# Optimization experiments

Measured on AMD Instinct MI355X. Metric: run time of the kernel, lower is better.

The kernel has to match this reference:

```python
import jax, jax.numpy as jnp
import numpy as np

N, L, T, F, H, E = 10000, 8, 16, 128, 256, 160000
NCONV = 3


def setup_inputs() -> dict:
    key = jax.random.key(0)
    ks = jax.random.split(key, 20)
    s = 0.05
    d = {}
    d['tree_inputs'] = jax.random.normal(ks[0], (N, L, F), jnp.float32)
    for i, name in enumerate(['seq2', 'seq3', 'seq4', 'seq5']):
        d[name] = jax.random.normal(ks[1 + i], (N, T, F), jnp.float32)
    d['edge_index'] = jax.random.randint(ks[5], (2, E), 0, N)
    d['tl_Wioux'] = jax.random.normal(ks[6], (3 * H, F)) * s
    d['tl_bioux'] = jnp.zeros((3 * H,))
    d['tl_Wiouh'] = jax.random.normal(ks[7], (3 * H, H)) * s
    d['tl_biouh'] = jnp.zeros((3 * H,))
    d['tl_Wfx'] = jax.random.normal(ks[8], (H, F)) * s
    d['tl_bfx'] = jnp.zeros((H,))
    d['tl_Wfh'] = jax.random.normal(ks[9], (H, H)) * s
    d['tl_bfh'] = jnp.zeros((H,))
    d['gru_Wih'] = jax.random.normal(ks[10], (4, 3 * H, F)) * s
    d['gru_Whh'] = jax.random.normal(ks[11], (4, 3 * H, H)) * s
    d['gru_bih'] = jnp.zeros((4, 3 * H))
    d['gru_bhh'] = jnp.zeros((4, 3 * H))
    d['comb_Wih'] = jax.random.normal(ks[12], (2, 3 * H, H)) * s
    d['comb_Whh'] = jax.random.normal(ks[13], (2, 3 * H, H)) * s
    d['comb_bih'] = jnp.zeros((2, 3 * H))
    d['comb_bhh'] = jnp.zeros((2, 3 * H))
    d['connect_W'] = jax.random.normal(ks[14], (H, 2 * 5 * H)) * s
    d['connect_b'] = jnp.zeros((H,))
    d['gcn_W'] = jax.random.normal(ks[15], (NCONV, H, H)) * s
    d['gcn_b'] = jnp.zeros((NCONV, H))
    return d


def _gru(x, Wih, Whh, bih, bhh, return_seq=False):
    # x: [N, T, F_in] -> last hidden [N, H] (or full seq [N, T, H])
    xg = jnp.einsum('ntf,gf->ntg', x, Wih) + bih  # precompute input projections
    h0 = jnp.zeros((x.shape[0], H), x.dtype)

    def step(h, xg_t):
        gh = h @ Whh.T + bhh
        r = jax.nn.sigmoid(xg_t[:, :H] + gh[:, :H])
        z = jax.nn.sigmoid(xg_t[:, H:2 * H] + gh[:, H:2 * H])
        n = jnp.tanh(xg_t[:, 2 * H:] + r * gh[:, 2 * H:])
        hn = (1.0 - z) * n + z * h
        return hn, (hn if return_seq else None)

    hT, ys = jax.lax.scan(step, h0, jnp.swapaxes(xg, 0, 1))
    return jnp.swapaxes(ys, 0, 1) if return_seq else hT


def reference(tree_inputs, seq2, seq3, seq4, seq5,
              tl_Wioux, tl_bioux, tl_Wiouh, tl_biouh, tl_Wfx, tl_bfx, tl_Wfh, tl_bfh,
              gru_Wih, gru_Whh, gru_bih, gru_bhh,
              comb_Wih, comb_Whh, comb_bih, comb_bhh,
              connect_W, connect_b, gcn_W, gcn_b, edge_index):
    # --- ChildSumTreeLSTM over chain trees (leaf -> root), vectorized over N trees ---
    xiou = jnp.einsum('nlf,gf->nlg', tree_inputs, tl_Wioux) + tl_bioux  # [N,L,3H]
    xf = jnp.einsum('nlf,hf->nlh', tree_inputs, tl_Wfx) + tl_bfx       # [N,L,H]

    def tstep(carry, inp):
        c, h = carry
        xiou_t, xf_t = inp
        iou = xiou_t + h @ tl_Wiouh.T + tl_biouh
        i = jax.nn.sigmoid(iou[:, :H])
        o = jax.nn.sigmoid(iou[:, H:2 * H])
        u = jnp.tanh(iou[:, 2 * H:])
        f = jax.nn.sigmoid(h @ tl_Wfh.T + tl_bfh + xf_t)
        c = i * u + f * c
        h = o * jnp.tanh(c)
        return (c, h), None

    c0 = jnp.zeros((N, H), tree_inputs.dtype)
    (_, feat1), _ = jax.lax.scan(tstep, (c0, c0), (jnp.swapaxes(xiou, 0, 1), jnp.swapaxes(xf, 0, 1)))

    # --- 4 unidirectional GRUs; keep last timestep (equal-length packed sequences) ---
    h2 = _gru(seq2, gru_Wih[0], gru_Whh[0], gru_bih[0], gru_bhh[0])
    h3 = _gru(seq3, gru_Wih[1], gru_Whh[1], gru_bih[1], gru_bhh[1])
    h4 = _gru(seq4, gru_Wih[2], gru_Whh[2], gru_bih[2], gru_bhh[2])
    h5 = _gru(seq5, gru_Wih[3], gru_Whh[3], gru_bih[3], gru_bhh[3])

    feats = jnp.stack([feat1, h2, h3, h4, h5], axis=1)  # [N,5,H]

    # --- bidirectional combine GRU ---
    out_f = _gru(feats, comb_Wih[0], comb_Whh[0], comb_bih[0], comb_bhh[0], return_seq=True)
    out_b = _gru(feats[:, ::-1, :], comb_Wih[1], comb_Whh[1], comb_bih[1], comb_bhh[1], return_seq=True)[:, ::-1, :]
    fv = jnp.concatenate([out_f, out_b], axis=-1).reshape(N, -1)  # [N, 5*2H]
    fv = fv @ connect_W.T + connect_b  # [N, H]  (dropout is identity at eval)

    # --- GCN layers (PyG GCNConv: add self-loops, symmetric norm) ---
    loops = jnp.arange(N)
    src = jnp.concatenate([edge_index[0], loops])
    dst = jnp.concatenate([edge_index[1], loops])
    deg = jax.ops.segment_sum(jnp.ones_like(src, fv.dtype), dst, num_segments=N)
    dinv = jax.lax.rsqrt(deg)  # deg >= 1 due to self-loops
    norm = dinv[src] * dinv[dst]

    def gcn(x, W, b):
        xw = x @ W.T
        agg = jax.ops.segment_sum(xw[src] * norm[:, None], dst, num_segments=N)
        return agg + b

    x = fv
    conv_output = x
    for i in range(NCONV):
        x = jax.nn.relu(gcn(x, gcn_W[i], gcn_b[i]))
        if i == NCONV - 1:
            # original code applies the last conv a second time for conv_output
            conv_output = jax.nn.relu(gcn(x, gcn_W[i], gcn_b[i]))

    pooled = jnp.max(conv_output, axis=0, keepdims=True)  # global max pool, single graph
    return pooled
```

## Files before the change

kernel.cpp:

```cpp
#include <hip/hip_runtime.h>
#include <math.h>

#define H 256
#define NROWS 10000
#define LTREE 8
#define TSEQ 16
#define FDIM 128
#define NE 160000
#define HTILE2 32768
#define XTILE 32768
#define H2 2621440
#define XZS 2621440

typedef __attribute__((ext_vector_type(8))) short short8;
typedef __attribute__((ext_vector_type(4))) float f32x4;
typedef unsigned short u16;

__device__ __forceinline__ u16 f2bf(float x) {
    unsigned int u = __float_as_uint(x);
    return (u16)((u + 0x7fffu + ((u >> 16) & 1u)) >> 16);
}
__device__ __forceinline__ float bf2f(u16 s) { return __uint_as_float(((unsigned int)s) << 16); }
__device__ __forceinline__ short8 ldf(const u16* __restrict__ p) { return *(const short8*)(p); }
__device__ __forceinline__ float fexp_(float x) { return __expf(fminf(x, 80.f)); }
__device__ __forceinline__ float fsig_(float x) { return 1.f / (1.f + fexp_(-x)); }
__device__ __forceinline__ float ftanh_(float x) {
    float e = fexp_(fmaxf(2.f * x, -80.f));
    return (e - 1.f) / (e + 1.f);
}
#define MFMA(A, B, C) C = __builtin_amdgcn_mfma_f32_16x16x32_bf16(A, B, C, 0, 0, 0)
#define MF2(AH, AL, BH, C) do { MFMA(AH, BH, C); MFMA(AL, BH, C); } while (0)

__device__ __forceinline__ void async16(u16* l, const u16* g) {
    __builtin_amdgcn_global_load_lds((__attribute__((address_space(1))) const void*)g,
                                     (__attribute__((address_space(3))) void*)l, 16, 0, 0);
}

__device__ __forceinline__ void xcd_swz(int& cbi, int& yy, int& zz) {
    const int gx = gridDim.x, gy = gridDim.y;
    int nwg8 = (gx * gy * gridDim.z) >> 3;
    int bid = blockIdx.x + gx * (blockIdx.y + gy * blockIdx.z);
    int wgid = (bid & 7) * nwg8 + (bid >> 3);
    cbi = wgid % gx;
    int rem = wgid / gx;
    yy = rem % gy;
    zz = rem / gy;
}

__device__ __forceinline__ size_t tpo128(int row, int g, int half) {
    return (size_t)(row >> 7) * XTILE + (size_t)(g >> 2) * 8192 +
           (size_t)((((g & 3) << 1) | half)) * 1024 + (size_t)(row & 127) * 8;
}
__device__ __forceinline__ size_t hpo(int row, int g) {
    return (size_t)(row >> 7) * HTILE2 + (size_t)g * 1024 + (size_t)(row & 127) * 8;
}

__device__ __forceinline__ void stageT(u16* ldsbuf, const u16* __restrict__ chunkbase,
                                       int w, int lane) {
#pragma unroll
    for (int cc = 0; cc < 4; cc++) {
        int eb = (w * 4 + cc) * 64;
        async16(ldsbuf + (size_t)eb * 8, chunkbase + (size_t)(eb + lane) * 8);
    }
}
__device__ __forceinline__ void stage64T(u16* ldsbuf, const u16* __restrict__ chunkbase,
                                         int w, int lane) {
#pragma unroll
    for (int cc = 0; cc < 2; cc++) {
        int p = w * 2 + cc;
        async16(ldsbuf + (size_t)p * 512, chunkbase + (size_t)p * 1024 + (size_t)lane * 8);
    }
}
__device__ __forceinline__ void stage_chunk64(u16* ldsbuf, const u16* __restrict__ src,
                                              int stride_u16, int kb_u16, int m0,
                                              int w, int lane) {
#pragma unroll
    for (int c = 0; c < 4; c++) {
        int e_base = (w * 4 + c) * 64;
        int e = e_base + lane;
        int p = e >> 6, rs = e & 63;
        int row = m0 + rs;
        if (row > NROWS - 1) row = NROWS - 1;
        const u16* g = src + (size_t)row * stride_u16 + kb_u16 + (p >> 1) * 16 + (p & 1) * 8;
        async16(ldsbuf + (size_t)e_base * 8, g);
    }
}

__device__ __forceinline__ void emit8t(u16* __restrict__ hi_p, u16* __restrict__ lo_p,
                                       const float* v8) {
    short8 h, l;
#pragma unroll
    for (int j = 0; j < 8; j++) {
        u16 hh = f2bf(v8[j]);
        h[j] = (short)hh;
        l[j] = (short)f2bf(v8[j] - bf2f(hh));
    }
    *(short8*)hi_p = h;
    *(short8*)(lo_p) = l;
}
__device__ __forceinline__ void emit8(u16* __restrict__ dst, const float* v8) {
    emit8t(dst, dst + 8, v8);
}
__global__ void k_splitWb(const float* __restrict__ src, u16* __restrict__ dst, int ngroups) {
    int g = blockIdx.x * 256 + threadIdx.x;
    if (g < ngroups) {
        float v[8];
        *(float4*)v = *(const float4*)(src + (size_t)g * 8);
        *(float4*)(v + 4) = *(const float4*)(src + (size_t)g * 8 + 4);
        short8 h;
#pragma unroll
        for (int j = 0; j < 8; j++) h[j] = (short)f2bf(v[j]);
        *(short8*)(dst + (size_t)g * 8) = h;
    }
}
__global__ void k_split_xseq(const float* __restrict__ s2, const float* __restrict__ s3,
                             const float* __restrict__ s4, const float* __restrict__ s5,
                             int t, u16* __restrict__ dst) {
    int bid = blockIdx.x;
    int xcd = bid & 7, chunk = bid >> 3;
    int z = xcd >> 1, half = xcd & 1;
    int g = chunk * 256 + threadIdx.x;
    int row = half * 5120 + (g >> 4);
    if (row >= NROWS) return;
    int gg = g & 15;
    const float* s = (z == 0) ? s2 : (z == 1) ? s3 : (z == 2) ? s4 : s5;
    const float* p = s + (size_t)row * (TSEQ * FDIM) + t * FDIM + gg * 8;
    float v[8];
    *(float4*)v = *(const float4*)p;
    *(float4*)(v + 4) = *(const float4*)(p + 4);
    u16* d = dst + (size_t)z * XZS;
    emit8t(d + tpo128(row, gg, 0), d + tpo128(row, gg, 1), v);
}
__global__ void k_split_xtree(const float* __restrict__ tree, int t, u16* __restrict__ dst) {
    int bid = blockIdx.x;
    int xcd = bid & 7, chunk = bid >> 3;
    int g = chunk * 256 + threadIdx.x;
    int row = xcd * 1280 + (g >> 4);
    if (row >= NROWS) return;
    int col = (g & 15) * 8;
    const float* p = tree + (size_t)row * (LTREE * FDIM) + t * FDIM + col;
    float v[8];
    *(float4*)v = *(const float4*)p;
    *(float4*)(v + 4) = *(const float4*)(p + 4);
    emit8(dst + (size_t)row * 256 + (size_t)(g & 15) * 16, v);
}
__global__ void k_splitNH2(const float* __restrict__ a, const float* __restrict__ b,
                           u16* __restrict__ dst) {
    int g = blockIdx.x * 256 + threadIdx.x;
    if (g < NROWS * 32) {
        float v[8];
        float4 x0 = *(const float4*)(a + (size_t)g * 8);
        float4 x1 = *(const float4*)(a + (size_t)g * 8 + 4);
        float4 y0 = *(const float4*)(b + (size_t)g * 8);
        float4 y1 = *(const float4*)(b + (size_t)g * 8 + 4);
        v[0] = x0.x + y0.x; v[1] = x0.y + y0.y; v[2] = x0.z + y0.z; v[3] = x0.w + y0.w;
        v[4] = x1.x + y1.x; v[5] = x1.y + y1.y; v[6] = x1.z + y1.z; v[7] = x1.w + y1.w;
        emit8(dst + (size_t)g * 16, v);
    }
}

template <int KX>
__global__ __launch_bounds__(256, 2) void k_rnn_step(
    const float* __restrict__ q0, const float* __restrict__ q1,
    const float* __restrict__ q2, const float* __restrict__ q3,
    int qoff4, u16* __restrict__ xnext,
    const u16* __restrict__ xp,
    const u16* __restrict__ Wih, long long wz,
    const u16* __restrict__ Whh, long long wzh,
    const float* __restrict__ bihB, const float* __restrict__ bhhB,
    const u16* __restrict__ hp,
    u16* __restrict__ op) {
    __shared__ u16 lds[2][8192];
    const int tid = threadIdx.x, lane = tid & 63, w = tid >> 6;
    const int lx = lane & 15, lg = lane >> 4;
    int cbi, yy, z;
    xcd_swz(cbi, yy, z);
    const int colw = cbi * 64 + w * 16;
    const int m0 = yy * 128;
    const u16* xb = xp + (size_t)z * XZS + (size_t)yy * XTILE;
    const u16* hb = hp + (size_t)z * H2;
    const u16* hbt = hb + (size_t)yy * HTILE2;
    const float* bih = bihB + z * 768;
    const float* bhh = bhhB + z * 768;
    constexpr int NCX = KX / 32;
    constexpr int NC = NCX + 4;

    const u16* bx0 = Wih + (size_t)z * wz + (size_t)(colw + lx) * KX + lg * 8;
    const u16* bx1 = bx0 + (size_t)256 * KX;
    const u16* bx2 = bx0 + (size_t)512 * KX;
    const u16* bh0 = Whh + (size_t)z * wzh + (size_t)(colw + lx) * 256 + lg * 8;
    const u16* bh1 = bh0 + 65536;
    const u16* bh2 = bh0 + 131072;

    const f32x4 zf = {0.f, 0.f, 0.f, 0.f};
    f32x4 aR[8], aZ[8], aNX[8], aNH[8];
#pragma unroll
    for (int rf = 0; rf < 8; rf++) { aR[rf] = zf; aZ[rf] = zf; aNX[rf] = zf; aNH[rf] = zf; }

    auto chunksrc = [&](int c) -> const u16* {
        return (c < NCX) ? xb + (size_t)c * 8192 : hbt + (size_t)(c - NCX) * 8192;
    };
    stageT(lds[0], chunksrc(0), w, lane);

    if (xnext) {
        const float* qs = (z == 0) ? q0 : (z == 1) ? q1 : (z == 2) ? q2 : q3;
        int row = m0 + (tid >> 1);
        if (row < NROWS) {
            int g0 = (cbi * 32 + (tid & 1) * 16) >> 3;
            const float* p = qs + (size_t)row * (TSEQ * FDIM) + qoff4 + g0 * 8;
            u16* d = xnext + (size_t)z * XZS;
            float v[8];
            *(float4*)v = *(const float4*)p;
            *(float4*)(v + 4) = *(const float4*)(p + 4);
            emit8t(d + tpo128(row, g0, 0), d + tpo128(row, g0, 1), v);
            *(float4*)v = *(const float4*)(p + 8);
            *(float4*)(v + 4) = *(const float4*)(p + 12);
            emit8t(d + tpo128(row, g0 + 1, 0), d + tpo128(row, g0 + 1, 1), v);
        }
    }

    for (int c = 0; c < NC; c++) {
        __syncthreads();
        if (c + 1 < NC) stageT(lds[(c + 1) & 1], chunksrc(c + 1), w, lane);
        const u16* lb = lds[c & 1];
        if (c < NCX) {
            short8 axh[8], axl[8];
            const u16* ph = lb + (size_t)(2 * lg) * 1024 + lx * 8;
#pragma unroll
            for (int rf = 0; rf < 8; rf++) {
                axh[rf] = ldf(ph + rf * 128);
                axl[rf] = ldf(ph + 1024 + rf * 128);
            }
            const int ko = c * 32;
            {
                short8 bh_ = ldf(bx0 + ko);
#pragma unroll
                for (int rf = 0; rf < 8; rf++) MF2(axh[rf], axl[rf], bh_, aR[rf]);
            }
            {
                short8 bh_ = ldf(bx1 + ko);
#pragma unroll
                for (int rf = 0; rf < 8; rf++) MF2(axh[rf], axl[rf], bh_, aZ[rf]);
            }
            {
                short8 bh_ = ldf(bx2 + ko);
#pragma unroll
                for (int rf = 0; rf < 8; rf++) MF2(axh[rf], axl[rf], bh_, aNX[rf]);
            }
        } else {
            const int cl = c - NCX;
#pragma unroll
            for (int s = 0; s < 2; s++) {
                short8 axh[8];
                const u16* ph = lb + (size_t)(s * 4 + lg) * 1024 + lx * 8;
#pragma unroll
                for (int rf = 0; rf < 8; rf++) axh[rf] = ldf(ph + rf * 128);
                const int ko = cl * 64 + s * 32;
                {
                    short8 bh_ = ldf(bh0 + ko);
#pragma unroll
                    for (int rf = 0; rf < 8; rf++) MFMA(axh[rf], bh_, aR[rf]);
                }
                {
                    short8 bh_ = ldf(bh1 + ko);
#pragma unroll
                    for (int rf = 0; rf < 8; rf++) MFMA(axh[rf], bh_, aZ[rf]);
                }
                {
                    short8 bh_ = ldf(bh2 + ko);
#pragma unroll
                    for (int rf = 0; rf < 8; rf++) MFMA(axh[rf], bh_, aNH[rf]);
                }
            }
        }
    }
    const int col = colw + lx;
    const float b_r = bih[col] + bhh[col];
    const float b_z = bih[256 + col] + bhh[256 + col];
    const float bx_n = bih[512 + col], bh_n = bhh[512 + col];
    const size_t colpart = (size_t)(col >> 3) * 1024 + (col & 7);
    u16* ob = op + (size_t)z * H2;
#pragma unroll
    for (int rf = 0; rf < 8; rf++) {
#pragma unroll
        for (int rr = 0; rr < 4; rr++) {
            int row = m0 + rf * 16 + lg * 4 + rr;
            if (row < NROWS) {
                float rg = fsig_(aR[rf][rr] + b_r);
                float zg = fsig_(aZ[rf][rr] + b_z);
                float ng = ftanh_(aNX[rf][rr] + bx_n + rg * (aNH[rf][rr] + bh_n));
                size_t addr = (size_t)(row >> 7) * HTILE2 + (size_t)(row & 127) * 8 + colpart;
                float hold = bf2f(hb[addr]);
                float hnew = (1.f - zg) * ng + zg * hold;
                ob[addr] = f2bf(hnew);
            }
        }
    }
}

__global__ __launch_bounds__(256, 3) void k_rnn_step64(
    const u16* __restrict__ xp, long long xo0, long long xo1,
    const u16* __restrict__ Wih, long long wz,
    const u16* __restrict__ Whh, long long wzh,
    const float* __restrict__ bihB, const float* __restrict__ bhhB,
    const u16* __restrict__ hp,
    u16* __restrict__ op) {
    __shared__ u16 lds[2][4096];
    const int tid = threadIdx.x, lane = tid & 63, w = tid >> 6;
    const int lx = lane & 15, lg = lane >> 4;
    int cbi, yy, z;
    xcd_swz(cbi, yy, z);
    const int colw = cbi * 64 + w * 16;
    const int m0 = yy * 64;
    const int tile = yy >> 1, rh = yy & 1;
    const u16* xb = xp + (size_t)((z == 1) ? xo1 : xo0) + (size_t)tile * HTILE2 + rh * 512;
    const u16* hb = hp + (size_t)z * H2;
    const u16* hbt = hb + (size_t)tile * HTILE2 + rh * 512;
    const float* bih = bihB + z * 768;
    const float* bhh = bhhB + z * 768;
    constexpr int NCX = 4, NC = 8;

    const u16* bx0 = Wih + (size_t)z * wz + (size_t)(colw + lx) * 256 + lg * 8;
    const u16* bx1 = bx0 + 65536;
    const u16* bx2 = bx0 + 131072;
    const u16* bh0 = Whh + (size_t)z * wzh + (size_t)(colw + lx) * 256 + lg * 8;
    const u16* bh1 = bh0 + 65536;
    const u16* bh2 = bh0 + 131072;

    const f32x4 zf = {0.f, 0.f, 0.f, 0.f};
    f32x4 aR[4], aZ[4], aNX[4], aNH[4];
#pragma unroll
    for (int rf = 0; rf < 4; rf++) { aR[rf] = zf; aZ[rf] = zf; aNX[rf] = zf; aNH[rf] = zf; }

    auto chunksrc = [&](int c) -> const u16* {
        return (c < NCX) ? xb + (size_t)c * 8192 : hbt + (size_t)(c - NCX) * 8192;
    };
    stage64T(lds[0], chunksrc(0), w, lane);

    for (int c = 0; c < NC; c++) {
        __syncthreads();
        if (c + 1 < NC) stage64T(lds[(c + 1) & 1], chunksrc(c + 1), w, lane);
        const u16* lb = lds[c & 1];
        const bool isX = (c < NCX);
        const int cl = isX ? c : c - NCX;
#pragma unroll
        for (int s = 0; s < 2; s++) {
            short8 axh[4];
            const u16* ph = lb + (size_t)(s * 4 + lg) * 512 + lx * 8;
#pragma unroll
            for (int rf = 0; rf < 4; rf++) axh[rf] = ldf(ph + rf * 128);
            const int ko = cl * 64 + s * 32;
            if (isX) {
                {
                    short8 bh_ = ldf(bx0 + ko);
#pragma unroll
                    for (int rf = 0; rf < 4; rf++) MFMA(axh[rf], bh_, aR[rf]);
                }
                {
                    short8 bh_ = ldf(bx1 + ko);
#pragma unroll
                    for (int rf = 0; rf < 4; rf++) MFMA(axh[rf], bh_, aZ[rf]);
                }
                {
                    short8 bh_ = ldf(bx2 + ko);
#pragma unroll
                    for (int rf = 0; rf < 4; rf++) MFMA(axh[rf], bh_, aNX[rf]);
                }
            } else {
                {
                    short8 bh_ = ldf(bh0 + ko);
#pragma unroll
                    for (int rf = 0; rf < 4; rf++) MFMA(axh[rf], bh_, aR[rf]);
                }
                {
                    short8 bh_ = ldf(bh1 + ko);
#pragma unroll
                    for (int rf = 0; rf < 4; rf++) MFMA(axh[rf], bh_, aZ[rf]);
                }
                {
                    short8 bh_ = ldf(bh2 + ko);
#pragma unroll
                    for (int rf = 0; rf < 4; rf++) MFMA(axh[rf], bh_, aNH[rf]);
                }
            }
        }
    }
    const int col = colw + lx;
    const float b_r = bih[col] + bhh[col];
    const float b_z = bih[256 + col] + bhh[256 + col];
    const float bx_n = bih[512 + col], bh_n = bhh[512 + col];
    const size_t colpart = (size_t)(col >> 3) * 1024 + (col & 7);
    u16* ob = op + (size_t)z * H2;
#pragma unroll
    for (int rf = 0; rf < 4; rf++) {
#pragma unroll
        for (int rr = 0; rr < 4; rr++) {
            int row = m0 + rf * 16 + lg * 4 + rr;
            if (row < NROWS) {
                float rg = fsig_(aR[rf][rr] + b_r);
                float zg = fsig_(aZ[rf][rr] + b_z);
                float ng = ftanh_(aNX[rf][rr] + bx_n + rg * (aNH[rf][rr] + bh_n));
                size_t addr = (size_t)(row >> 7) * HTILE2 + (size_t)(row & 127) * 8 + colpart;
                float hold = bf2f(hb[addr]);
                float hnew = (1.f - zg) * ng + zg * hold;
                ob[addr] = f2bf(hnew);
            }
        }
    }
}

__global__ __launch_bounds__(256, 3) void k_tree_step_mf(
    const float* __restrict__ treenext, u16* __restrict__ xtnext,
    const u16* __restrict__ txp,
    const u16* __restrict__ Wx, const u16* __restrict__ Wh,
    const u16* __restrict__ Wfx, const u16* __restrict__ Wfh,
    const float* __restrict__ bioux, const float* __restrict__ biouh,
    const float* __restrict__ bfx, const float* __restrict__ bfh,
    const u16* __restrict__ hp, float* __restrict__ cst,
    u16* __restrict__ op, int tiledOut) {
    __shared__ u16 lds[2][8192];
    const int tid = threadIdx.x, lane = tid & 63, w = tid >> 6;
    const int lx = lane & 15, lg = lane >> 4;
    int cbi, yy, zz;
    xcd_swz(cbi, yy, zz);
    const int colw = cbi * 64 + w * 16;
    const int m0 = yy * 64;
    constexpr int NCX = 2, NC = 6;

    const u16* bx0 = Wx + (size_t)(colw + lx) * 128 + lg * 8;
    const u16* bx1 = bx0 + 32768;
    const u16* bx2 = bx0 + 65536;
    const u16* bxf = Wfx + (size_t)(colw + lx) * 128 + lg * 8;
    const u16* bh0 = Wh + (size_t)(colw + lx) * 256 + lg * 8;
    const u16* bh1 = bh0 + 65536;
    const u16* bh2 = bh0 + 131072;
    const u16* bhf = Wfh + (size_t)(colw + lx) * 256 + lg * 8;

    const f32x4 zf = {0.f, 0.f, 0.f, 0.f};
    f32x4 aI[4], aO[4], aU[4], aF[4];
#pragma unroll
    for (int rf = 0; rf < 4; rf++) { aI[rf] = zf; aO[rf] = zf; aU[rf] = zf; aF[rf] = zf; }

    stage_chunk64(lds[0], txp, 256, 0, m0, w, lane);

    if (xtnext) {
        int row = m0 + (tid >> 2);
        if (row < NROWS) {
            int c0 = cbi * 32 + (tid & 3) * 8;
            const float* p = treenext + (size_t)row * (LTREE * FDIM) + c0;
            float v[8];
            *(float4*)v = *(const float4*)p;
            *(float4*)(v + 4) = *(const float4*)(p + 4);
            emit8(xtnext + (size_t)row * 256 + (size_t)(c0 >> 3) * 16, v);
        }
    }

    for (int c = 0; c < NC; c++) {
        __syncthreads();
        if (c + 1 < NC) {
            u16* nb = lds[(c + 1) & 1];
            if (c + 1 < NCX) stage_chunk64(nb, txp, 256, (c + 1) * 128, m0, w, lane);
            else stage_chunk64(nb, hp, 512, (c + 1 - NCX) * 128, m0, w, lane);
        }
        const u16* lb = lds[c & 1];
        const bool isX = (c < NCX);
        const int cl = isX ? c : c - NCX;
#pragma unroll
        for (int s = 0; s < 2; s++) {
            short8 axh[4], axl[4];
            const u16* ph = lb + (size_t)(2 * (s * 4 + lg)) * 512 + lx * 8;
#pragma unroll
            for (int rf = 0; rf < 4; rf++) {
                axh[rf] = ldf(ph + rf * 128);
                axl[rf] = ldf(ph + 512 + rf * 128);
            }
            const int ko = cl * 64 + s * 32;
            const u16* p0 = isX ? bx0 : bh0;
            const u16* p1 = isX ? bx1 : bh1;
            const u16* p2 = isX ? bx2 : bh2;
            const u16* p3 = isX ? bxf : bhf;
            {
                short8 bh_ = ldf(p0 + ko);
#pragma unroll
                for (int rf = 0; rf < 4; rf++) MF2(axh[rf], axl[rf], bh_, aI[rf]);
            }
            {
                short8 bh_ = ldf(p1 + ko);
#pragma unroll
                for (int rf = 0; rf < 4; rf++) MF2(axh[rf], axl[rf], bh_, aO[rf]);
            }
            {
                short8 bh_ = ldf(p2 + ko);
#pragma unroll
                for (int rf = 0; rf < 4; rf++) MF2(axh[rf], axl[rf], bh_, aU[rf]);
            }
            {
                short8 bh_ = ldf(p3 + ko);
#pragma unroll
                for (int rf = 0; rf < 4; rf++) MF2(axh[rf], axl[rf], bh_, aF[rf]);
            }
        }
    }
    const int col = colw + lx;
    const float b_i = bioux[col] + biouh[col];
    const float b_o = bioux[256 + col] + biouh[256 + col];
    const float b_u = bioux[512 + col] + biouh[512 + col];
    const float b_f = bfx[col] + bfh[col];
    const int cpo = ((col >> 3) << 4) + (col & 7);
    const size_t colpart2 = (size_t)(col >> 3) * 1024 + (col & 7);
#pragma unroll
    for (int rf = 0; rf < 4; rf++) {
#pragma unroll
        for (int rr = 0; rr < 4; rr++) {
            int row = m0 + rf * 16 + lg * 4 + rr;
            if (row < NROWS) {
                float ig = fsig_(aI[rf][rr] + b_i);
                float og = fsig_(aO[rf][rr] + b_o);
                float ug = ftanh_(aU[rf][rr] + b_u);
                float fg = fsig_(aF[rf][rr] + b_f);
                size_t ci = (size_t)row * H + col;
                float cnew = ig * ug + fg * cst[ci];
                cst[ci] = cnew;
                float hnew = og * ftanh_(cnew);
                if (tiledOut) {
                    size_t addr = (size_t)(row >> 7) * HTILE2 + (size_t)(row & 127) * 8 + colpart2;
                    op[addr] = f2bf(hnew);
                } else {
                    u16 hh = f2bf(hnew);
                    size_t oi = (size_t)row * 512 + cpo;
                    op[oi] = hh;
                    op[oi + 8] = f2bf(hnew - bf2f(hh));
                }
            }
        }
    }
}

__global__ __launch_bounds__(256) void k_fv_acc_mf(
    float* __restrict__ fvbase, const u16* __restrict__ hq,
    const u16* __restrict__ Wc, int off_f, int off_b) {
    const int tid = threadIdx.x, lane = tid & 63, w = tid >> 6;
    const int lx = lane & 15, kl8 = (lane >> 4);
    int cbi, yy, z;
    xcd_swz(cbi, yy, z);
    const int wr = w >> 1, wc = w & 1;
    const int cb = cbi * 64 + wc * 32;
    const int m0 = yy * 128 + wr * 64;
    int arow[4];
#pragma unroll
    for (int rf = 0; rf < 4; rf++) {
        int r = m0 + rf * 16 + lx;
        arow[rf] = (r < NROWS) ? r : NROWS - 1;
    }
    const f32x4 zf = {0.f, 0.f, 0.f, 0.f};
    f32x4 acc[4][2] = {{zf, zf}, {zf, zf}, {zf, zf}, {zf, zf}};
    const u16* aB = hq + (size_t)z * H2;
    const int off = z ? off_b : off_f;
    const u16* a[4];
#pragma unroll
    for (int rf = 0; rf < 4; rf++) {
        a[rf] = aB + (size_t)(arow[rf] >> 7) * HTILE2 + (size_t)(arow[rf] & 127) * 8 +
                (size_t)kl8 * 1024;
    }
    const u16* bp0 = Wc + (size_t)(cb + lx) * 2560 + off + kl8 * 8;
    const u16* bp1 = bp0 + 16 * 2560;
#pragma unroll
    for (int it = 0; it < 8; it++) {
        short8 axh[4];
#pragma unroll
        for (int rf = 0; rf < 4; rf++) {
            axh[rf] = ldf(a[rf]);
            a[rf] += 4096;
        }
        const int kb = it * 32;
        {
            short8 bh = ldf(bp0 + kb);
#pragma unroll
            for (int rf = 0; rf < 4; rf++) MFMA(axh[rf], bh, acc[rf][0]);
        }
        {
            short8 bh = ldf(bp1 + kb);
#pragma unroll
            for (int rf = 0; rf < 4; rf++) MFMA(axh[rf], bh, acc[rf][1]);
        }
    }
    float* fv = fvbase + (size_t)z * (NROWS * H);
#pragma unroll
    for (int rf = 0; rf < 4; rf++) {
#pragma unroll
        for (int cf = 0; cf < 2; cf++) {
            int col = cb + cf * 16 + lx;
#pragma unroll
            for (int rr = 0; rr < 4; rr++) {
                int row = m0 + rf * 16 + (lane >> 4) * 4 + rr;
                if (row < NROWS) fv[(size_t)row * H + col] += acc[rf][cf][rr];
            }
        }
    }
}

__global__ __launch_bounds__(256) void k_gcn_gemm(
    float* __restrict__ out, const u16* __restrict__ ap_, const u16* __restrict__ W) {
    const int tid = threadIdx.x, lane = tid & 63, w = tid >> 6;
    const int lx = lane & 15, kl = (lane >> 4) * 8;
    int cbi, yy, zz;
    xcd_swz(cbi, yy, zz);
    const int cb = cbi * 64, m0 = yy * 128 + w * 32;
    int arow[2];
#pragma unroll
    for (int rf = 0; rf < 2; rf++) {
        int r = m0 + rf * 16 + lx;
        arow[rf] = (r < NROWS) ? r : NROWS - 1;
    }
    const f32x4 zf = {0.f, 0.f, 0.f, 0.f};
    f32x4 acc[2][4] = {{zf, zf, zf, zf}, {zf, zf, zf, zf}};
    const u16* a0 = ap_ + (size_t)arow[0] * 512 + kl * 2;
    const u16* a1 = ap_ + (size_t)arow[1] * 512 + kl * 2;
    const u16* bp0 = W + (size_t)(cb + lx) * 256 + kl;
    const u16* bp1 = bp0 + 16 * 256;
    const u16* bp2 = bp0 + 32 * 256;
    const u16* bp3 = bp0 + 48 * 256;
#pragma unroll
    for (int kb = 0; kb < 256; kb += 32) {
        short8 axh[2], axl[2];
        axh[0] = ldf(a0 + kb * 2); axl[0] = ldf(a0 + kb * 2 + 8);
        axh[1] = ldf(a1 + kb * 2); axl[1] = ldf(a1 + kb * 2 + 8);
        {
            short8 bh = ldf(bp0 + kb);
#pragma unroll
            for (int rf = 0; rf < 2; rf++) MF2(axh[rf], axl[rf], bh, acc[rf][0]);
        }
        {
            short8 bh = ldf(bp1 + kb);
#pragma unroll
            for (int rf = 0; rf < 2; rf++) MF2(axh[rf], axl[rf], bh, acc[rf][1]);
        }
        {
            short8 bh = ldf(bp2 + kb);
#pragma unroll
            for (int rf = 0; rf < 2; rf++) MF2(axh[rf], axl[rf], bh, acc[rf][2]);
        }
        {
            short8 bh = ldf(bp3 + kb);
#pragma unroll
            for (int rf = 0; rf < 2; rf++) MF2(axh[rf], axl[rf], bh, acc[rf][3]);
        }
    }
#pragma unroll
    for (int rf = 0; rf < 2; rf++) {
#pragma unroll
        for (int cf = 0; cf < 4; cf++) {
            int col = cb + cf * 16 + lx;
#pragma unroll
            for (int rr = 0; rr < 4; rr++) {
                int row = m0 + rf * 16 + (lane >> 4) * 4 + rr;
                if (row < NROWS) out[(size_t)row * H + col] = acc[rf][cf][rr];
            }
        }
    }
}

__global__ void k_fv_init(float* fv, const float* __restrict__ b) {
    int idx = blockIdx.x * 256 + threadIdx.x;
    if (idx < NROWS * H) fv[idx] = b[idx & (H - 1)];
}
__global__ void k_cnt(int* __restrict__ cnt, const int* __restrict__ dst) {
    int i = blockIdx.x * 256 + threadIdx.x;
    if (i < NE) atomicAdd(&cnt[dst[i]], 1);
}
__global__ void k_scan(const int* __restrict__ cnt, int* __restrict__ rowptr) {
    __shared__ int part[256];
    int tid = threadIdx.x;
    int st = tid * 40, en = (st + 40 > NROWS) ? NROWS : st + 40;
    int s = 0;
    for (int i = st; i < en; i++) s += cnt[i];
    part[tid] = s;
    __syncthreads();
    if (tid == 0) {
        int run = 0;
        for (int i = 0; i < 256; i++) { int t = part[i]; part[i] = run; run += t; }
        rowptr[NROWS] = run;
    }
    __syncthreads();
    int run = part[tid];
    for (int i = st; i < en; i++) { rowptr[i] = run; run += cnt[i]; }
}
__global__ void k_dinv(float* __restrict__ dinv, const int* __restrict__ cnt) {
    int i = blockIdx.x * 256 + threadIdx.x;
    if (i < NROWS) dinv[i] = rsqrtf(1.0f + (float)cnt[i]);
}
__global__ void k_fill(int* __restrict__ csr, int* __restrict__ cursor,
                       const int* __restrict__ rowptr, const int* __restrict__ ei) {
    int e = blockIdx.x * 256 + threadIdx.x;
    if (e < NE) {
        int d = ei[NE + e];
        int p = atomicAdd(&cursor[d], 1);
        csr[rowptr[d] + p] = ei[e];
    }
}
__global__ __launch_bounds__(256) void k_gather(
    float* __restrict__ out, u16* __restrict__ xcp,
    const float* __restrict__ xw, const float* __restrict__ dinv,
    const int* __restrict__ rowptr, const int* __restrict__ csr, const float* __restrict__ b) {
    int node = blockIdx.x * 4 + (threadIdx.x >> 6);
    if (node >= NROWS) return;
    int lane = threadIdx.x & 63;
    float dn = dinv[node];
    float4 acc = *(const float4*)(xw + (size_t)node * H + lane * 4);
    float dn2 = dn * dn;
    acc.x *= dn2; acc.y *= dn2; acc.z *= dn2; acc.w *= dn2;
    int e0 = rowptr[node], e1 = rowptr[node + 1];
    for (int i = e0; i < e1; i++) {
        int s = csr[i];
        float wgt = dn * dinv[s];
        const float4 v = *(const float4*)(xw + (size_t)s * H + lane * 4);
        acc.x += v.x * wgt; acc.y += v.y * wgt; acc.z += v.z * wgt; acc.w += v.w * wgt;
    }
    const float4 bv = *(const float4*)(b + lane * 4);
    float o[4];
    o[0] = fmaxf(acc.x + bv.x, 0.f);
    o[1] = fmaxf(acc.y + bv.y, 0.f);
    o[2] = fmaxf(acc.z + bv.z, 0.f);
    o[3] = fmaxf(acc.w + bv.w, 0.f);
    *(float4*)(out + (size_t)node * H + lane * 4) = *(const float4*)o;
    u16 hs[4], ls[4];
#pragma unroll
    for (int j = 0; j < 4; j++) {
        hs[j] = f2bf(o[j]);
        ls[j] = f2bf(o[j] - bf2f(hs[j]));
    }
    size_t bidx = (size_t)node * 512 + (size_t)(lane >> 1) * 16 + (lane & 1) * 4;
    *(short4*)(xcp + bidx) = *(const short4*)hs;
    *(short4*)(xcp + bidx + 8) = *(const short4*)ls;
}
__global__ void k_colmax(float* __restrict__ out, const float* __restrict__ x) {
    int j = threadIdx.x;
    float m = 0.0f;
    for (int r = blockIdx.x; r < NROWS; r += gridDim.x)
        m = fmaxf(m, x[(size_t)r * H + j]);
    atomicMax((int*)&out[j], __float_as_int(m));
}

extern "C" void kernel_launch(void* const* d_in, const int* in_sizes, int n_in,
                              void* d_out, int out_size, void* d_ws, size_t ws_size,
                              hipStream_t stream) {
    const float* tree = (const float*)d_in[0];
    const float* s2 = (const float*)d_in[1];
    const float* s3 = (const float*)d_in[2];
    const float* s4 = (const float*)d_in[3];
    const float* s5 = (const float*)d_in[4];
    const int* edge = (const int*)d_in[5];
    const float* tl_Wioux = (const float*)d_in[6];
    const float* tl_bioux = (const float*)d_in[7];
    const float* tl_Wiouh = (const float*)d_in[8];
    const float* tl_biouh = (const float*)d_in[9];
    const float* tl_Wfx = (const float*)d_in[10];
    const float* tl_bfx = (const float*)d_in[11];
    const float* tl_Wfh = (const float*)d_in[12];
    const float* tl_bfh = (const float*)d_in[13];
    const float* gru_Wih = (const float*)d_in[14];
    const float* gru_Whh = (const float*)d_in[15];
    const float* gru_bih = (const float*)d_in[16];
    const float* gru_bhh = (const float*)d_in[17];
    const float* comb_Wih = (const float*)d_in[18];
    const float* comb_Whh = (const float*)d_in[19];
    const float* comb_bih = (const float*)d_in[20];
    const float* comb_bhh = (const float*)d_in[21];
    const float* connect_W = (const float*)d_in[22];
    const float* connect_b = (const float*)d_in[23];
    const float* gcn_W = (const float*)d_in[24];
    const float* gcn_b = (const float*)d_in[25];

    char* base = (char*)d_ws;
    size_t off = 0;
    auto aus = [&](size_t nu16) { u16* p = (u16*)(base + off); off += nu16 * sizeof(u16); return p; };
    u16* tx = aus(98304);
    u16* th = aus(196608);
    u16* tfx = aus(32768);
    u16* tfh = aus(65536);
    u16* gWih = aus(393216);
    u16* gWhh = aus(786432);
    u16* cWih = aus(393216);
    u16* cWhh = aus(393216);
    u16* cn = aus(655360);
    u16* gc = aus(196608);
    u16* feats = aus((size_t)5 * H2);
    u16* hA = aus((size_t)4 * H2);
    u16* hB = aus((size_t)4 * H2);
    u16* SA = aus((size_t)4 * XZS);
    u16* SB = aus((size_t)4 * XZS);

    const dim3 blk(256);

    hipMemsetAsync(d_out, 0, H * sizeof(float), stream);

    auto SPW = [&](const float* s, u16* d, int n) {
        k_splitWb<<<(n / 8 + 255) / 256, blk, 0, stream>>>(s, d, n / 8);
    };
    SPW(tl_Wioux, tx, 98304);
    SPW(tl_Wiouh, th, 196608);
    SPW(tl_Wfx, tfx, 32768);
    SPW(tl_Wfh, tfh, 65536);
    SPW(gru_Wih, gWih, 393216);
    SPW(gru_Whh, gWhh, 786432);
    SPW(comb_Wih, cWih, 393216);
    SPW(comb_Whh, cWhh, 393216);
    SPW(connect_W, cn, 655360);
    SPW(gcn_W, gc, 196608);

    float* cbuf = (float*)SA;
    u16* xtA = SA + 5120000;
    u16* xtB = SA + 7680000;
    hipMemsetAsync(hA, 0, (size_t)NROWS * 512 * 2, stream);
    hipMemsetAsync(cbuf, 0, (size_t)NROWS * H * 4, stream);
    k_split_xtree<<<640, blk, 0, stream>>>(tree, 0, xtA);
    {
        u16 *p = hA, *q = hB;
        for (int t = 0; t < LTREE; ++t) {
            bool last = (t == LTREE - 1);
            u16* xin = (t & 1) ? xtB : xtA;
            u16* xnx = last ? (u16*)0 : ((t & 1) ? xtA : xtB);
            k_tree_step_mf<<<dim3(4, 160, 1), blk, 0, stream>>>(
                tree + (t + 1) * FDIM, xnx,
                xin, tx, th, tfx, tfh, tl_bioux, tl_biouh, tl_bfx, tl_bfh,
                p, cbuf, last ? feats : q, last ? 1 : 0);
            u16* tmp = p; p = q; q = tmp;
        }
    }

    u16* xsA = SA;
    u16* xsB = SB;
    hipMemsetAsync(hA, 0, (size_t)4 * H2 * 2, stream);
    k_split_xseq<<<2560, blk, 0, stream>>>(s2, s3, s4, s5, 0, xsA);
    {
        u16 *p = hA, *q = hB;
        for (int t = 0; t < TSEQ; ++t) {
            bool last = (t == TSEQ - 1);
            u16* xin = (t & 1) ? xsB : xsA;
            u16* xnx = last ? (u16*)0 : ((t & 1) ? xsA : xsB);
            k_rnn_step<128><<<dim3(4, 80, 4), blk, 0, stream>>>(
                s2, s3, s4, s5, (t + 1) * FDIM, xnx,
                xin,
                gWih, 98304LL, gWhh, 196608LL, gru_bih, gru_bhh,
                p,
                last ? feats + H2 : q);
            u16* tmp = p; p = q; q = tmp;
        }
    }

    float* fvF = (float*)SA;
    float* fvB = fvF + (size_t)NROWS * H;
    hipMemsetAsync(hA, 0, (size_t)2 * H2 * 2, stream);
    k_fv_init<<<(NROWS * H + 255) / 256, blk, 0, stream>>>(fvF, connect_b);
    hipMemsetAsync(fvB, 0, (size_t)NROWS * H * 4, stream);
    {
        u16 *p = hA, *q = hB;
        for (int s = 0; s < 5; ++s) {
            k_rnn_step64<<<dim3(4, 160, 2), blk, 0, stream>>>(
                feats, (long long)s * H2, (long long)(4 - s) * H2,
                cWih, 196608LL, cWhh, 196608LL, comb_bih, comb_bhh,
                p, q);
            k_fv_acc_mf<<<dim3(4, 79, 2), blk, 0, stream>>>(
                fvF, q, cn, s * 512, (4 - s) * 512 + 256);
            u16* tmp = p; p = q; q = tmp;
        }
    }

    int* cnt = (int*)(hB + 6000000);
    int* rowptr = cnt + 10016;
    int* cursor = rowptr + 10016;
    int* csr = cursor + 10016;
    float* dinv = (float*)(csr + NE);
    hipMemsetAsync(cnt, 0, NROWS * sizeof(int), stream);
    hipMemsetAsync(cursor, 0, NROWS * sizeof(int), stream);
    k_cnt<<<(NE + 255) / 256, blk, 0, stream>>>(cnt, edge + NE);
    k_scan<<<1, blk, 0, stream>>>(cnt, rowptr);
    k_dinv<<<(NROWS + 255) / 256, blk, 0, stream>>>(dinv, cnt);
    k_fill<<<(NE + 255) / 256, blk, 0, stream>>>(csr, cursor, rowptr, edge);

    {
        u16* xc = hB;
        float* xw = (float*)SB;
        float* cur = fvF;
        float* nxt = (float*)hA;
        k_splitNH2<<<1250, blk, 0, stream>>>(fvF, fvB, xc);
        for (int i = 0; i < 4; ++i) {
            int wi = (i < 3) ? i : 2;
            k_gcn_gemm<<<dim3(4, 80, 1), blk, 0, stream>>>(xw, xc, gc + (size_t)wi * 65536);
            k_gather<<<(NROWS + 3) / 4, blk, 0, stream>>>(nxt, xc, xw, dinv, rowptr, csr,
                                                          gcn_b + wi * H);
            float* tmp = cur; cur = nxt; nxt = tmp;
        }
        k_colmax<<<256, blk, 0, stream>>>((float*)d_out, cur);
    }
}
```

Before: 1.932 ms.

## Drop split-bf16 hi/lo activation encoding, use single bf16 operands everywhere

Removes the hi+lo two-term bf16 representation of activations (x inputs, tree hidden state, GCN inputs), which doubled MFMA count and operand bytes for those products. Buffers, layouts, staging helpers and the MFMA loops are rewritten for a single bf16 term, halving the chunk count for input projections and the memory traffic for these activations. The cost is lower precision in the matmuls, which may push results closer to or past the tolerance.

```diff
diff --git a/kernel.cpp b/kernel.cpp
--- a/kernel.cpp
+++ b/kernel.cpp
@@ -8,9 +8,9 @@
 #define FDIM 128
 #define NE 160000
 #define HTILE2 32768
-#define XTILE 32768
+#define XT2 16384
 #define H2 2621440
-#define XZS 2621440
+#define XZ2 1310720
 
 typedef __attribute__((ext_vector_type(8))) short short8;
 typedef __attribute__((ext_vector_type(4))) float f32x4;
@@ -29,7 +29,6 @@
     return (e - 1.f) / (e + 1.f);
 }
 #define MFMA(A, B, C) C = __builtin_amdgcn_mfma_f32_16x16x32_bf16(A, B, C, 0, 0, 0)
-#define MF2(AH, AL, BH, C) do { MFMA(AH, BH, C); MFMA(AL, BH, C); } while (0)
 
 __device__ __forceinline__ void async16(u16* l, const u16* g) {
     __builtin_amdgcn_global_load_lds((__attribute__((address_space(1))) const void*)g,
@@ -47,12 +46,8 @@
     zz = rem / gy;
 }
 
-__device__ __forceinline__ size_t tpo128(int row, int g, int half) {
-    return (size_t)(row >> 7) * XTILE + (size_t)(g >> 2) * 8192 +
-           (size_t)((((g & 3) << 1) | half)) * 1024 + (size_t)(row & 127) * 8;
-}
-__device__ __forceinline__ size_t hpo(int row, int g) {
-    return (size_t)(row >> 7) * HTILE2 + (size_t)g * 1024 + (size_t)(row & 127) * 8;
+__device__ __forceinline__ size_t xpo(int row, int g) {
+    return (size_t)(row >> 7) * XT2 + (size_t)g * 1024 + (size_t)(row & 127) * 8;
 }
 
 __device__ __forceinline__ void stageT(u16* ldsbuf, const u16* __restrict__ chunkbase,
@@ -71,9 +66,9 @@
         async16(ldsbuf + (size_t)p * 512, chunkbase + (size_t)p * 1024 + (size_t)lane * 8);
     }
 }
-__device__ __forceinline__ void stage_chunk64(u16* ldsbuf, const u16* __restrict__ src,
-                                              int stride_u16, int kb_u16, int m0,
-                                              int w, int lane) {
+__device__ __forceinline__ void stage_chunk64h(u16* ldsbuf, const u16* __restrict__ src,
+                                               int stride_u16, int kb_u16, int m0,
+                                               int w, int lane) {
 #pragma unroll
     for (int c = 0; c < 4; c++) {
         int e_base = (w * 4 + c) * 64;
@@ -81,25 +76,16 @@
         int p = e >> 6, rs = e & 63;
         int row = m0 + rs;
         if (row > NROWS - 1) row = NROWS - 1;
-        const u16* g = src + (size_t)row * stride_u16 + kb_u16 + (p >> 1) * 16 + (p & 1) * 8;
+        const u16* g = src + (size_t)row * stride_u16 + kb_u16 + p * 8;
         async16(ldsbuf + (size_t)e_base * 8, g);
     }
 }
 
-__device__ __forceinline__ void emit8t(u16* __restrict__ hi_p, u16* __restrict__ lo_p,
-                                       const float* v8) {
-    short8 h, l;
-#pragma unroll
-    for (int j = 0; j < 8; j++) {
-        u16 hh = f2bf(v8[j]);
-        h[j] = (short)hh;
-        l[j] = (short)f2bf(v8[j] - bf2f(hh));
-    }
-    *(short8*)hi_p = h;
-    *(short8*)(lo_p) = l;
-}
-__device__ __forceinline__ void emit8(u16* __restrict__ dst, const float* v8) {
-    emit8t(dst, dst + 8, v8);
+__device__ __forceinline__ void emit8h(u16* __restrict__ dst, const float* v8) {
+    short8 h;
+#pragma unroll
+    for (int j = 0; j < 8; j++) h[j] = (short)f2bf(v8[j]);
+    *(short8*)dst = h;
 }
 __global__ void k_splitWb(const float* __restrict__ src, u16* __restrict__ dst, int ngroups) {
     int g = blockIdx.x * 256 + threadIdx.x;
@@ -107,10 +93,7 @@
         float v[8];
         *(float4*)v = *(const float4*)(src + (size_t)g * 8);
         *(float4*)(v + 4) = *(const float4*)(src + (size_t)g * 8 + 4);
-        short8 h;
-#pragma unroll
-        for (int j = 0; j < 8; j++) h[j] = (short)f2bf(v[j]);
-        *(short8*)(dst + (size_t)g * 8) = h;
+        emit8h(dst + (size_t)g * 8, v);
     }
 }
 __global__ void k_split_xseq(const float* __restrict__ s2, const float* __restrict__ s3,
@@ -128,8 +111,7 @@
     float v[8];
     *(float4*)v = *(const float4*)p;
     *(float4*)(v + 4) = *(const float4*)(p + 4);
-    u16* d = dst + (size_t)z * XZS;
-    emit8t(d + tpo128(row, gg, 0), d + tpo128(row, gg, 1), v);
+    emit8h(dst + (size_t)z * XZ2 + xpo(row, gg), v);
 }
 __global__ void k_split_xtree(const float* __restrict__ tree, int t, u16* __restrict__ dst) {
     int bid = blockIdx.x;
@@ -142,7 +124,7 @@
     float v[8];
     *(float4*)v = *(const float4*)p;
     *(float4*)(v + 4) = *(const float4*)(p + 4);
-    emit8(dst + (size_t)row * 256 + (size_t)(g & 15) * 16, v);
+    emit8h(dst + (size_t)row * 128 + col, v);
 }
 __global__ void k_splitNH2(const float* __restrict__ a, const float* __restrict__ b,
                            u16* __restrict__ dst) {
@@ -155,11 +137,10 @@
         float4 y1 = *(const float4*)(b + (size_t)g * 8 + 4);
         v[0] = x0.x + y0.x; v[1] = x0.y + y0.y; v[2] = x0.z + y0.z; v[3] = x0.w + y0.w;
         v[4] = x1.x + y1.x; v[5] = x1.y + y1.y; v[6] = x1.z + y1.z; v[7] = x1.w + y1.w;
-        emit8(dst + (size_t)g * 16, v);
-    }
-}
-
-template <int KX>
+        emit8h(dst + (size_t)g * 8, v);
+    }
+}
+
 __global__ __launch_bounds__(256, 2) void k_rnn_step(
     const float* __restrict__ q0, const float* __restrict__ q1,
     const float* __restrict__ q2, const float* __restrict__ q3,
@@ -177,17 +158,16 @@
     xcd_swz(cbi, yy, z);
     const int colw = cbi * 64 + w * 16;
     const int m0 = yy * 128;
-    const u16* xb = xp + (size_t)z * XZS + (size_t)yy * XTILE;
+    const u16* xb = xp + (size_t)z * XZ2 + (size_t)yy * XT2;
     const u16* hb = hp + (size_t)z * H2;
     const u16* hbt = hb + (size_t)yy * HTILE2;
     const float* bih = bihB + z * 768;
     const float* bhh = bhhB + z * 768;
-    constexpr int NCX = KX / 32;
-    constexpr int NC = NCX + 4;
-
-    const u16* bx0 = Wih + (size_t)z * wz + (size_t)(colw + lx) * KX + lg * 8;
-    const u16* bx1 = bx0 + (size_t)256 * KX;
-    const u16* bx2 = bx0 + (size_t)512 * KX;
+    constexpr int NCX = 2, NC = 6;
+
+    const u16* bx0 = Wih + (size_t)z * wz + (size_t)(colw + lx) * 128 + lg * 8;
+    const u16* bx1 = bx0 + 32768;
+    const u16* bx2 = bx0 + 65536;
     const u16* bh0 = Whh + (size_t)z * wzh + (size_t)(colw + lx) * 256 + lg * 8;
     const u16* bh1 = bh0 + 65536;
     const u16* bh2 = bh0 + 131072;
@@ -208,14 +188,14 @@
         if (row < NROWS) {
             int g0 = (cbi * 32 + (tid & 1) * 16) >> 3;
             const float* p = qs + (size_t)row * (TSEQ * FDIM) + qoff4 + g0 * 8;
-            u16* d = xnext + (size_t)z * XZS;
+            u16* d = xnext + (size_t)z * XZ2;
             float v[8];
             *(float4*)v = *(const float4*)p;
             *(float4*)(v + 4) = *(const float4*)(p + 4);
-            emit8t(d + tpo128(row, g0, 0), d + tpo128(row, g0, 1), v);
+            emit8h(d + xpo(row, g0), v);
             *(float4*)v = *(const float4*)(p + 8);
             *(float4*)(v + 4) = *(const float4*)(p + 12);
-            emit8t(d + tpo128(row, g0 + 1, 0), d + tpo128(row, g0 + 1, 1), v);
+            emit8h(d + xpo(row, g0 + 1), v);
         }
     }
 
@@ -223,39 +203,32 @@
         __syncthreads();
         if (c + 1 < NC) stageT(lds[(c + 1) & 1], chunksrc(c + 1), w, lane);
         const u16* lb = lds[c & 1];
-        if (c < NCX) {
-            short8 axh[8], axl[8];
-            const u16* ph = lb + (size_t)(2 * lg) * 1024 + lx * 8;
-#pragma unroll
-            for (int rf = 0; rf < 8; rf++) {
-                axh[rf] = ldf(ph + rf * 128);
-                axl[rf] = ldf(ph + 1024 + rf * 128);
-            }
-            const int ko = c * 32;
-            {
-                short8 bh_ = ldf(bx0 + ko);
-#pragma unroll
-                for (int rf = 0; rf < 8; rf++) MF2(axh[rf], axl[rf], bh_, aR[rf]);
-            }
-            {
-                short8 bh_ = ldf(bx1 + ko);
-#pragma unroll
-                for (int rf = 0; rf < 8; rf++) MF2(axh[rf], axl[rf], bh_, aZ[rf]);
-            }
-            {
-                short8 bh_ = ldf(bx2 + ko);
-#pragma unroll
-                for (int rf = 0; rf < 8; rf++) MF2(axh[rf], axl[rf], bh_, aNX[rf]);
-            }
-        } else {
-            const int cl = c - NCX;
-#pragma unroll
-            for (int s = 0; s < 2; s++) {
-                short8 axh[8];
-                const u16* ph = lb + (size_t)(s * 4 + lg) * 1024 + lx * 8;
-#pragma unroll
-                for (int rf = 0; rf < 8; rf++) axh[rf] = ldf(ph + rf * 128);
-                const int ko = cl * 64 + s * 32;
+        const bool isX = (c < NCX);
+        const int cl = isX ? c : c - NCX;
+#pragma unroll
+        for (int s = 0; s < 2; s++) {
+            short8 axh[8];
+            const u16* ph = lb + (size_t)(s * 4 + lg) * 1024 + lx * 8;
+#pragma unroll
+            for (int rf = 0; rf < 8; rf++) axh[rf] = ldf(ph + rf * 128);
+            const int ko = cl * 64 + s * 32;
+            if (isX) {
+                {
+                    short8 bh_ = ldf(bx0 + ko);
+#pragma unroll
+                    for (int rf = 0; rf < 8; rf++) MFMA(axh[rf], bh_, aR[rf]);
+                }
+                {
+                    short8 bh_ = ldf(bx1 + ko);
+#pragma unroll
+                    for (int rf = 0; rf < 8; rf++) MFMA(axh[rf], bh_, aZ[rf]);
+                }
+                {
+                    short8 bh_ = ldf(bx2 + ko);
+#pragma unroll
+                    for (int rf = 0; rf < 8; rf++) MFMA(axh[rf], bh_, aNX[rf]);
+                }
+            } else {
                 {
                     short8 bh_ = ldf(bh0 + ko);
 #pragma unroll
@@ -425,7 +398,7 @@
     xcd_swz(cbi, yy, zz);
     const int colw = cbi * 64 + w * 16;
     const int m0 = yy * 64;
-    constexpr int NCX = 2, NC = 6;
+    constexpr int NC = 3;
 
     const u16* bx0 = Wx + (size_t)(colw + lx) * 128 + lg * 8;
     const u16* bx1 = bx0 + 32768;
@@ -441,7 +414,7 @@
 #pragma unroll
     for (int rf = 0; rf < 4; rf++) { aI[rf] = zf; aO[rf] = zf; aU[rf] = zf; aF[rf] = zf; }
 
-    stage_chunk64(lds[0], txp, 256, 0, m0, w, lane);
+    stage_chunk64h(lds[0], txp, 128, 0, m0, w, lane);
 
     if (xtnext) {
         int row = m0 + (tid >> 2);
@@ -451,30 +424,22 @@
             float v[8];
             *(float4*)v = *(const float4*)p;
             *(float4*)(v + 4) = *(const float4*)(p + 4);
-            emit8(xtnext + (size_t)row * 256 + (size_t)(c0 >> 3) * 16, v);
+            emit8h(xtnext + (size_t)row * 128 + c0, v);
         }
     }
 
     for (int c = 0; c < NC; c++) {
         __syncthreads();
-        if (c + 1 < NC) {
-            u16* nb = lds[(c + 1) & 1];
-            if (c + 1 < NCX) stage_chunk64(nb, txp, 256, (c + 1) * 128, m0, w, lane);
-            else stage_chunk64(nb, hp, 512, (c + 1 - NCX) * 128, m0, w, lane);
-        }
+        if (c + 1 < NC) stage_chunk64h(lds[(c + 1) & 1], hp, 256, c * 128, m0, w, lane);
         const u16* lb = lds[c & 1];
-        const bool isX = (c < NCX);
-        const int cl = isX ? c : c - NCX;
-#pragma unroll
-        for (int s = 0; s < 2; s++) {
-            short8 axh[4], axl[4];
-            const u16* ph = lb + (size_t)(2 * (s * 4 + lg)) * 512 + lx * 8;
-#pragma unroll
-            for (int rf = 0; rf < 4; rf++) {
-                axh[rf] = ldf(ph + rf * 128);
-                axl[rf] = ldf(ph + 512 + rf * 128);
-            }
-            const int ko = cl * 64 + s * 32;
+        const bool isX = (c == 0);
+#pragma unroll
+        for (int s = 0; s < 4; s++) {
+            short8 axh[4];
+            const u16* ph = lb + (size_t)(s * 4 + lg) * 512 + lx * 8;
+#pragma unroll
+            for (int rf = 0; rf < 4; rf++) axh[rf] = ldf(ph + rf * 128);
+            const int ko = isX ? s * 32 : (c - 1) * 128 + s * 32;
             const u16* p0 = isX ? bx0 : bh0;
             const u16* p1 = isX ? bx1 : bh1;
             const u16* p2 = isX ? bx2 : bh2;
@@ -482,22 +447,22 @@
             {
                 short8 bh_ = ldf(p0 + ko);
 #pragma unroll
-                for (int rf = 0; rf < 4; rf++) MF2(axh[rf], axl[rf], bh_, aI[rf]);
+                for (int rf = 0; rf < 4; rf++) MFMA(axh[rf], bh_, aI[rf]);
             }
             {
                 short8 bh_ = ldf(p1 + ko);
 #pragma unroll
-                for (int rf = 0; rf < 4; rf++) MF2(axh[rf], axl[rf], bh_, aO[rf]);
+                for (int rf = 0; rf < 4; rf++) MFMA(axh[rf], bh_, aO[rf]);
             }
             {
                 short8 bh_ = ldf(p2 + ko);
 #pragma unroll
-                for (int rf = 0; rf < 4; rf++) MF2(axh[rf], axl[rf], bh_, aU[rf]);
+                for (int rf = 0; rf < 4; rf++) MFMA(axh[rf], bh_, aU[rf]);
             }
             {
                 short8 bh_ = ldf(p3 + ko);
 #pragma unroll
-                for (int rf = 0; rf < 4; rf++) MF2(axh[rf], axl[rf], bh_, aF[rf]);
+                for (int rf = 0; rf < 4; rf++) MFMA(axh[rf], bh_, aF[rf]);
             }
         }
     }
@@ -506,7 +471,6 @@
     const float b_o = bioux[256 + col] + biouh[256 + col];
     const float b_u = bioux[512 + col] + biouh[512 + col];
     const float b_f = bfx[col] + bfh[col];
-    const int cpo = ((col >> 3) << 4) + (col & 7);
     const size_t colpart2 = (size_t)(col >> 3) * 1024 + (col & 7);
 #pragma unroll
     for (int rf = 0; rf < 4; rf++) {
@@ -526,10 +490,7 @@
                     size_t addr = (size_t)(row >> 7) * HTILE2 + (size_t)(row & 127) * 8 + colpart2;
                     op[addr] = f2bf(hnew);
                 } else {
-                    u16 hh = f2bf(hnew);
-                    size_t oi = (size_t)row * 512 + cpo;
-                    op[oi] = hh;
-                    op[oi + 8] = f2bf(hnew - bf2f(hh));
+                    op[(size_t)row * 256 + col] = f2bf(hnew);
                 }
             }
         }
@@ -614,36 +575,36 @@
     }
     const f32x4 zf = {0.f, 0.f, 0.f, 0.f};
     f32x4 acc[2][4] = {{zf, zf, zf, zf}, {zf, zf, zf, zf}};
-    const u16* a0 = ap_ + (size_t)arow[0] * 512 + kl * 2;
-    const u16* a1 = ap_ + (size_t)arow[1] * 512 + kl * 2;
+    const u16* a0 = ap_ + (size_t)arow[0] * 256 + kl;
+    const u16* a1 = ap_ + (size_t)arow[1] * 256 + kl;
     const u16* bp0 = W + (size_t)(cb + lx) * 256 + kl;
     const u16* bp1 = bp0 + 16 * 256;
     const u16* bp2 = bp0 + 32 * 256;
     const u16* bp3 = bp0 + 48 * 256;
 #pragma unroll
     for (int kb = 0; kb < 256; kb += 32) {
-        short8 axh[2], axl[2];
-        axh[0] = ldf(a0 + kb * 2); axl[0] = ldf(a0 + kb * 2 + 8);
-        axh[1] = ldf(a1 + kb * 2); axl[1] = ldf(a1 + kb * 2 + 8);
+        short8 axh[2];
+        axh[0] = ldf(a0 + kb);
+        axh[1] = ldf(a1 + kb);
         {
             short8 bh = ldf(bp0 + kb);
 #pragma unroll
-            for (int rf = 0; rf < 2; rf++) MF2(axh[rf], axl[rf], bh, acc[rf][0]);
+            for (int rf = 0; rf < 2; rf++) MFMA(axh[rf], bh, acc[rf][0]);
         }
         {
             short8 bh = ldf(bp1 + kb);
 #pragma unroll
-            for (int rf = 0; rf < 2; rf++) MF2(axh[rf], axl[rf], bh, acc[rf][1]);
+            for (int rf = 0; rf < 2; rf++) MFMA(axh[rf], bh, acc[rf][1]);
         }
         {
             short8 bh = ldf(bp2 + kb);
 #pragma unroll
-            for (int rf = 0; rf < 2; rf++) MF2(axh[rf], axl[rf], bh, acc[rf][2]);
+            for (int rf = 0; rf < 2; rf++) MFMA(axh[rf], bh, acc[rf][2]);
         }
         {
             short8 bh = ldf(bp3 + kb);
 #pragma unroll
-            for (int rf = 0; rf < 2; rf++) MF2(axh[rf], axl[rf], bh, acc[rf][3]);
+            for (int rf = 0; rf < 2; rf++) MFMA(axh[rf], bh, acc[rf][3]);
         }
     }
 #pragma unroll
@@ -723,15 +684,10 @@
     o[2] = fmaxf(acc.z + bv.z, 0.f);
     o[3] = fmaxf(acc.w + bv.w, 0.f);
     *(float4*)(out + (size_t)node * H + lane * 4) = *(const float4*)o;
-    u16 hs[4], ls[4];
-#pragma unroll
-    for (int j = 0; j < 4; j++) {
-        hs[j] = f2bf(o[j]);
-        ls[j] = f2bf(o[j] - bf2f(hs[j]));
-    }
-    size_t bidx = (size_t)node * 512 + (size_t)(lane >> 1) * 16 + (lane & 1) * 4;
-    *(short4*)(xcp + bidx) = *(const short4*)hs;
-    *(short4*)(xcp + bidx + 8) = *(const short4*)ls;
+    u16 hs[4];
+#pragma unroll
+    for (int j = 0; j < 4; j++) hs[j] = f2bf(o[j]);
+    *(short4*)(xcp + (size_t)node * 256 + lane * 4) = *(const short4*)hs;
 }
 __global__ void k_colmax(float* __restrict__ out, const float* __restrict__ x) {
     int j = threadIdx.x;
@@ -787,8 +743,8 @@
     u16* feats = aus((size_t)5 * H2);
     u16* hA = aus((size_t)4 * H2);
     u16* hB = aus((size_t)4 * H2);
-    u16* SA = aus((size_t)4 * XZS);
-    u16* SB = aus((size_t)4 * XZS);
+    u16* SA = aus((size_t)8 * XZ2);
+    u16* SB = aus((size_t)8 * XZ2);
 
     const dim3 blk(256);
 
@@ -810,8 +766,8 @@
 
     float* cbuf = (float*)SA;
     u16* xtA = SA + 5120000;
-    u16* xtB = SA + 7680000;
-    hipMemsetAsync(hA, 0, (size_t)NROWS * 512 * 2, stream);
+    u16* xtB = SA + 6400000;
+    hipMemsetAsync(hA, 0, (size_t)NROWS * 256 * 2, stream);
     hipMemsetAsync(cbuf, 0, (size_t)NROWS * H * 4, stream);
     k_split_xtree<<<640, blk, 0, stream>>>(tree, 0, xtA);
     {
@@ -838,7 +794,7 @@
             bool last = (t == TSEQ - 1);
             u16* xin = (t & 1) ? xsB : xsA;
             u16* xnx = last ? (u16*)0 : ((t & 1) ? xsA : xsB);
-            k_rnn_step<128><<<dim3(4, 80, 4), blk, 0, stream>>>(
+            k_rnn_step<<<dim3(4, 80, 4), blk, 0, stream>>>(
                 s2, s3, s4, s5, (t + 1) * FDIM, xnx,
                 xin,
                 gWih, 98304LL, gWhh, 196608LL, gru_bih, gru_bhh,
```

After: 1.832 ms. -5.2%, faster.
